# Kernel tuning notes

Hardware: AMD Instinct MI355X
Metric: run time of the kernel (lower is better)

The kernel has to match this reference:

```python
import jax, jax.numpy as jnp
import numpy as np
import math

D_HEAD = 64  # scaling uses sqrt(d_head), NOT sqrt of full projection dim (faithful to source)

def setup_inputs() -> dict:
    key = jax.random.key(0)
    ks = jax.random.split(key, 9)
    B, S, D = 4, 2048, 1024
    s = 0.02
    return {
        "x": jax.random.normal(ks[0], (B, S, D), dtype=jnp.float32),
        "Wq": jax.random.normal(ks[1], (D, D), dtype=jnp.float32) * s,
        "bq": jax.random.normal(ks[2], (D,), dtype=jnp.float32) * s,
        "Wk": jax.random.normal(ks[3], (D, D), dtype=jnp.float32) * s,
        "bk": jax.random.normal(ks[4], (D,), dtype=jnp.float32) * s,
        "Wv": jax.random.normal(ks[5], (D, D), dtype=jnp.float32) * s,
        "bv": jax.random.normal(ks[6], (D,), dtype=jnp.float32) * s,
        "Wo": jax.random.normal(ks[7], (D, D), dtype=jnp.float32) * s,
        "bo": jax.random.normal(ks[8], (D,), dtype=jnp.float32) * s,
    }

def reference(x, Wq, bq, Wk, bk, Wv, bv, Wo, bo):
    # Q/K/V projections: [B,S,D] @ [D,D] + b
    Q = jnp.einsum('bsd,de->bse', x, Wq) + bq
    K = jnp.einsum('bsd,de->bse', x, Wk) + bk
    V = jnp.einsum('bsd,de->bse', x, Wv) + bv
    # NOTE: source does bmm over the FULL projected dim (no head split),
    # scaled by sqrt(d_head) only.
    scores = jnp.einsum('bqd,bkd->bqk', Q, K) / math.sqrt(D_HEAD)  # [B,S,S]
    S_len = scores.shape[-1]
    causal = jnp.tril(jnp.ones((S_len, S_len), dtype=bool))
    scores = jnp.where(causal, scores, -jnp.inf)
    weights = jax.nn.softmax(scores, axis=-1)
    attn_out = jnp.einsum('bqk,bkd->bqd', weights, V)
    return jnp.einsum('bsd,de->bse', attn_out, Wo) + bo
```

## Files before the change

### kernel.cpp

```cpp
#include <hip/hip_runtime.h>
#include <stdint.h>

typedef _Float16 f16;
typedef __attribute__((ext_vector_type(8))) _Float16 f16x8;
typedef __attribute__((ext_vector_type(4))) _Float16 f16x4;
typedef __attribute__((ext_vector_type(4))) float f32x4;

typedef __attribute__((address_space(3))) uint32_t lds_u32;
typedef const __attribute__((address_space(1))) uint32_t glb_u32;

__device__ __forceinline__ void gload_lds16(const void* g, void* l) {
    __builtin_amdgcn_global_load_lds((glb_u32*)g, (lds_u32*)l, 16, 0, 0);
}


template<int ROWS>
__device__ __forceinline__
void stage2(const f16* __restrict__ G, int ldg, f16* lds,
            int grow0, int k0, int tid)
{
    const int l = tid & 63, w = tid >> 6;
    #pragma unroll
    for (int q = 0; q < ROWS / 32; ++q) {
        const int r = q * 32 + w * 8 + (l >> 3);
        const int csw = (((l & 7) ^ (r & 7)) << 3);
        gload_lds16(G + (long long)(grow0 + r) * ldg + (k0 + csw),
                    lds + q * 2048 + w * 512);
    }
}

template<int OUT_MODE, int CAUSAL, int TM, int TN>
__device__ __forceinline__
void gemm2_body(const f16* __restrict__ A, const f16* __restrict__ B,
                const float* __restrict__ bias, void* __restrict__ Cv,
                int M, int N, int K,
                long long sAb, long long sBb, long long sCb, float scale,
                int bx, int by, int bzi)
{
    constexpr int IM = TM / 32;
    constexpr int JN = TN / 32;

    int mtile, n0;
    if (CAUSAL == 1) {
        int rem = bx, mi = 0;
        while (rem > mi) { rem -= mi + 1; ++mi; }
        mtile = mi;
        n0 = rem * TN;
    } else {
        mtile = by;
        n0 = bx * TN;
    }

    const int tid  = threadIdx.x;
    const int wave = tid >> 6;
    const int lane = tid & 63;
    const long long bz = bzi;
    A += bz * sAb;
    B += bz * sBb;

    __shared__ f16 As[2][TM * 64];
    __shared__ f16 Bs[2][TN * 64];

    const int fr  = lane & 15;
    const int hk  = lane >> 4;
    const int lsw = lane & 7;
    const int wm  = (wave >> 1) * (TM / 2);
    const int wn  = (wave & 1) * (TN / 2);

    const int npass = (CAUSAL == 2) ? 2 : 1;
    for (int pass = 0; pass < npass; ++pass) {
        const int mt = (CAUSAL == 2 && pass == 1) ? (M / TM - 1 - mtile) : mtile;
        const int m0 = mt * TM;
        const int Kend = (CAUSAL == 2) ? (m0 + TM) : K;

        f32x4 acc[IM][JN] = {};

        stage2<TM>(A, K, &As[0][0], m0, 0, tid);
        stage2<TN>(B, K, &Bs[0][0], n0, 0, tid);
        asm volatile("s_waitcnt vmcnt(0)" ::: "memory");
        __builtin_amdgcn_s_barrier();

        int cur = 0;
        for (int k0 = 0; k0 < Kend; k0 += 64) {
            if (k0 + 64 < Kend) {
                stage2<TM>(A, K, &As[cur ^ 1][0], m0, k0 + 64, tid);
                stage2<TN>(B, K, &Bs[cur ^ 1][0], n0, k0 + 64, tid);
            }

            f16x8 af[IM][2], bf[JN][2];
            #pragma unroll
            for (int i = 0; i < IM; ++i)
                #pragma unroll
                for (int kk = 0; kk < 2; ++kk)
                    af[i][kk] = *(const f16x8*)((const char*)&As[cur][0] +
                        ((wm + i * 16 + fr) << 7) +
                        ((((kk << 2) | hk) ^ lsw) << 4));
            #pragma unroll
            for (int j = 0; j < JN; ++j)
                #pragma unroll
                for (int kk = 0; kk < 2; ++kk)
                    bf[j][kk] = *(const f16x8*)((const char*)&Bs[cur][0] +
                        ((wn + j * 16 + fr) << 7) +
                        ((((kk << 2) | hk) ^ lsw) << 4));

            asm volatile("s_waitcnt lgkmcnt(0)" ::: "memory");
            __builtin_amdgcn_s_setprio(1);
            #pragma unroll
            for (int i = 0; i < IM; ++i)
                #pragma unroll
                for (int j = 0; j < JN; ++j)
                    #pragma unroll
                    for (int kk = 0; kk < 2; ++kk)
                        acc[i][j] = __builtin_amdgcn_mfma_f32_16x16x32_f16(
                            af[i][kk], bf[j][kk], acc[i][j], 0, 0, 0);
            __builtin_amdgcn_s_setprio(0);

            asm volatile("s_waitcnt vmcnt(0)" ::: "memory");
            __builtin_amdgcn_s_barrier();
            cur ^= 1;
        }

        const int cn = lane & 15;
        const int cm = (lane >> 4) * 4;
        #pragma unroll
        for (int j = 0; j < JN; ++j) {
            const int gn = n0 + wn + j * 16 + cn;
            #pragma unroll
            for (int i = 0; i < IM; ++i) {
                const int gm = m0 + wm + i * 16 + cm;
                if (OUT_MODE == 0) {
                    const float bv = bias ? bias[gn] : 0.f;
                    float* C = (float*)Cv + bz * sCb;
                    #pragma unroll
                    for (int r = 0; r < 4; ++r)
                        C[(long long)(gm + r) * N + gn] = acc[i][j][r] * scale + bv;
                } else {
                    const float bv = bias ? bias[(long long)bz * N + gn] : 0.f;
                    f16* C = (f16*)Cv + bz * sCb;
                    #pragma unroll
                    for (int r = 0; r < 4; ++r)
                        C[(long long)(gm + r) * N + gn] = (f16)(acc[i][j][r] * scale + bv);
                }
            }
        }
    }
}

template<int OUT_MODE, int CAUSAL, int TM, int TN>
__global__ __launch_bounds__(256, 2)
void gemm2_bt(const f16* __restrict__ A, const f16* __restrict__ B,
              const float* __restrict__ bias, void* __restrict__ Cv,
              int M, int N, int K,
              long long sAb, long long sBb, long long sCb, float scale)
{
    gemm2_body<OUT_MODE, CAUSAL, TM, TN>(A, B, bias, Cv, M, N, K,
                                         sAb, sBb, sCb, scale,
                                         blockIdx.x, blockIdx.y, blockIdx.z);
}


__device__ __forceinline__
void stage_half(const f16* __restrict__ G, int ldg, f16* lds_half,
                int grow0, int k0, int tid)
{
    const int lr  = tid >> 3;
    const int csw = ((tid & 7) * 8) ^ ((lr & 7) << 3);
    gload_lds16(G + (long long)(grow0 + lr) * ldg + (k0 + csw),
                lds_half + ((tid >> 6) << 9));
    gload_lds16(G + (long long)(grow0 + 64 + lr) * ldg + (k0 + csw),
                lds_half + 4096 + ((tid >> 6) << 9));
}

template<int MODE>
__global__ __launch_bounds__(512, 2)
void gemm256_4ph(const f16* __restrict__ A, const f16* __restrict__ B,
                 const float* __restrict__ bias, const float* __restrict__ bias2,
                 f16* __restrict__ C0, f16* __restrict__ C1,
                 int M, int N, int K,
                 long long sAb, long long sBb, long long sCb, float scale)
{
    __shared__ f16 As[2][16384];
    __shared__ f16 Bs[2][16384];

    const int nwg  = gridDim.x;
    const int orig = blockIdx.x;
    const int swz  = (orig & 7) * (nwg >> 3) + (orig >> 3);

    int m0, n0;
    long long bz = 0;
    if (MODE == 1) {
        const int nr  = M >> 8;
        const int per = nr * (nr + 1) / 2;
        bz = swz / per;
        int rem = swz - (int)bz * per, mi = 0;
        while (rem > mi) { rem -= mi + 1; ++mi; }
        m0 = mi << 8;
        n0 = rem << 8;
    } else {
        const int ntn = N >> 8;
        const int mt = swz / ntn, nt = swz - mt * ntn;
        m0 = mt << 8;
        n0 = nt << 8;
    }
    A += bz * sAb;
    B += bz * sBb;

    const int tid  = threadIdx.x;
    const int lane = tid & 63;
    const int wave = tid >> 6;
    const int wm = (wave >> 2) << 7;
    const int wn = (wave & 3) << 6;
    const int fr  = lane & 15;
    const int hk  = lane >> 4;
    const int lsw = lane & 7;
    const int nkt = K >> 6;

    f32x4 acc[8][4] = {};
    f16x8 bf[4][2];

    stage_half(A, K, &As[0][0],    m0,       0, tid);
    stage_half(A, K, &As[0][8192], m0 + 128, 0, tid);
    stage_half(B, K, &Bs[0][0],    n0,       0, tid);
    stage_half(B, K, &Bs[0][8192], n0 + 128, 0, tid);
    if (nkt > 1) {
        stage_half(B, K, &Bs[1][0],    n0,       64, tid);
        stage_half(B, K, &Bs[1][8192], n0 + 128, 64, tid);
        asm volatile("s_waitcnt vmcnt(4)" ::: "memory");
    } else {
        asm volatile("s_waitcnt vmcnt(0)" ::: "memory");
    }
    __builtin_amdgcn_s_barrier();

    for (int t = 0; t < nkt; ++t) {
        const f16* Ab = As[t & 1];
        const f16* Bb = Bs[t & 1];
        #pragma unroll
        for (int p = 0; p < 4; ++p) {
            if (p == 0) {
                #pragma unroll
                for (int j = 0; j < 4; ++j)
                    #pragma unroll
                    for (int kk = 0; kk < 2; ++kk)
                        bf[j][kk] = *(const f16x8*)((const char*)Bb +
                            ((wn + j * 16 + fr) << 7) +
                            ((((kk << 2) | hk) ^ lsw) << 4));
            }
            f16x8 af[2][2];
            #pragma unroll
            for (int ii = 0; ii < 2; ++ii)
                #pragma unroll
                for (int kk = 0; kk < 2; ++kk)
                    af[ii][kk] = *(const f16x8*)((const char*)Ab +
                        ((wm + (2 * p + ii) * 16 + fr) << 7) +
                        ((((kk << 2) | hk) ^ lsw) << 4));

            if (p == 0 && t + 1 < nkt)
                stage_half(A, K, &As[(t + 1) & 1][0],    m0,       (t + 1) << 6, tid);
            if (p == 1 && t + 1 < nkt)
                stage_half(A, K, &As[(t + 1) & 1][8192], m0 + 128, (t + 1) << 6, tid);
            if (p == 2 && t + 2 < nkt)
                stage_half(B, K, &Bs[t & 1][0],          n0,       (t + 2) << 6, tid);
            if (p == 3 && t + 2 < nkt)
                stage_half(B, K, &Bs[t & 1][8192],       n0 + 128, (t + 2) << 6, tid);

            if (p == 0) asm volatile("s_waitcnt lgkmcnt(8)" ::: "memory");
            __builtin_amdgcn_s_barrier();
            asm volatile("s_waitcnt lgkmcnt(0)" ::: "memory");
            __builtin_amdgcn_s_setprio(1);
            #pragma unroll
            for (int ii = 0; ii < 2; ++ii)
                #pragma unroll
                for (int j = 0; j < 4; ++j)
                    #pragma unroll
                    for (int kk = 0; kk < 2; ++kk)
                        acc[2 * p + ii][j] = __builtin_amdgcn_mfma_f32_16x16x32_f16(
                            af[ii][kk], bf[j][kk], acc[2 * p + ii][j], 0, 0, 0);
            __builtin_amdgcn_s_setprio(0);
            if (p == 3) {
                if (t + 2 < nkt) asm volatile("s_waitcnt vmcnt(4)" ::: "memory");
                else             asm volatile("s_waitcnt vmcnt(0)" ::: "memory");
            }
            __builtin_amdgcn_s_barrier();
        }
    }

    const int cn  = lane & 15;
    const int cm4 = (lane >> 4) * 4;
    #pragma unroll
    for (int j = 0; j < 4; ++j) {
        const int gn = n0 + wn + j * 16 + cn;
        if (MODE == 3) {
            const int sel = gn >> 10;
            const int nn  = gn & 1023;
            #pragma unroll
            for (int i = 0; i < 8; ++i) {
                const int gm = m0 + wm + i * 16 + cm4;
                if (sel == 0) {
                    #pragma unroll
                    for (int r = 0; r < 4; ++r)
                        C0[(long long)(gm + r) * 1024 + nn] = (f16)acc[i][j][r];
                } else {
                    const float bb = bias2[nn];
                    const int b = gm >> 11, s = gm & 2047;
                    f16x4 pk;
                    #pragma unroll
                    for (int r = 0; r < 4; ++r)
                        pk[r] = (f16)(acc[i][j][r] + bb);
                    *(f16x4*)&C1[(long long)b * 2097152 + (long long)nn * 2048 + s] = pk;
                }
            }
        } else {
            const float cbv = bias ? bias[bz * N + gn] : 0.f;
            f16* Cc = C0 + bz * sCb;
            #pragma unroll
            for (int i = 0; i < 8; ++i) {
                const int gm = m0 + wm + i * 16 + cm4;
                #pragma unroll
                for (int r = 0; r < 4; ++r)
                    Cc[(long long)(gm + r) * N + gn] = (f16)(acc[i][j][r] * scale + cbv);
            }
        }
    }
}

__global__ __launch_bounds__(256)
void prep(const float* __restrict__ x,  const float* __restrict__ Wq,
          const float* __restrict__ bq, const float* __restrict__ Wk,
          const float* __restrict__ Wv, const float* __restrict__ bv,
          const float* __restrict__ Wo,
          f16* __restrict__ xb,  f16* __restrict__ Wqf, f16* __restrict__ Wkf,
          f16* __restrict__ Wvf, f16* __restrict__ Wot,
          float* __restrict__ bvo, float* __restrict__ wvec)
{
    __shared__ f16 tile[32][33];
    __shared__ float red[4][64];
    const int t = threadIdx.x;
    int id = blockIdx.x;

    if (id < 8192) {
        const int i = (id * 256 + t) * 4;
        const float4 v = *(const float4*)&x[i];
        f16x4 o; o[0]=(f16)v.x; o[1]=(f16)v.y; o[2]=(f16)v.z; o[3]=(f16)v.w;
        *(f16x4*)&xb[i] = o;
        return;
    }
    id -= 8192;
    if (id < 3072) {
        const float* src = (id < 1024) ? Wq : (id < 2048) ? Wk : Wv;
        f16* dst = (id < 1024) ? Wqf : (id < 2048) ? Wkf : Wvf;
        const int i = ((id & 1023) * 256 + t) * 4;
        const float4 v = *(const float4*)&src[i];
        f16x4 o; o[0]=(f16)v.x; o[1]=(f16)v.y; o[2]=(f16)v.z; o[3]=(f16)v.w;
        *(f16x4*)&dst[i] = o;
        return;
    }
    id -= 3072;
    if (id < 1024) {
        const int bx = (id & 31) * 32, by = (id >> 5) * 32;
        const int tx = t & 31, ty = t >> 5;
        #pragma unroll
        for (int i = 0; i < 32; i += 8)
            tile[ty + i][tx] = (f16)Wo[(long long)(by + ty + i) * 1024 + (bx + tx)];
        __syncthreads();
        #pragma unroll
        for (int i = 0; i < 32; i += 8)
            Wot[(long long)(bx + ty + i) * 1024 + (by + tx)] = tile[tx][ty + i];
        return;
    }
    id -= 1024;
    if (id < 16) {
        const int e0 = id * 64;
        const int wave = t >> 6, lane = t & 63;
        float a0 = 0.f, a1 = 0.f, a2 = 0.f, a3 = 0.f;
        for (int i = 0; i < 256; i += 4) {
            const int k = wave * 256 + i;
            a0 += bv[k]     * Wo[(long long)k * 1024 + e0 + lane];
            a1 += bv[k + 1] * Wo[(long long)(k + 1) * 1024 + e0 + lane];
            a2 += bv[k + 2] * Wo[(long long)(k + 2) * 1024 + e0 + lane];
            a3 += bv[k + 3] * Wo[(long long)(k + 3) * 1024 + e0 + lane];
        }
        red[wave][lane] = (a0 + a1) + (a2 + a3);
        __syncthreads();
        if (wave == 0)
            bvo[e0 + lane] = red[0][lane] + red[1][lane] + red[2][lane] + red[3][lane];
        return;
    }
    id -= 16;
    {
        const int row = id * 4 + (t >> 6);
        const int lane = t & 63;
        const float* src = Wk + (long long)row * 1024;
        float a = 0.f;
        #pragma unroll
        for (int tt = 0; tt < 16; ++tt) a += src[lane + 64 * tt] * bq[lane + 64 * tt];
        #pragma unroll
        for (int o = 32; o > 0; o >>= 1) a += __shfl_down(a, o);
        if (lane == 0) wvec[row] = a * 0.125f;
    }
}

__global__ __launch_bounds__(256, 2)
void dual_weights_cvec(const f16* __restrict__ Wkf, const f16* __restrict__ Wqf,
                       const f16* __restrict__ Wot, const f16* __restrict__ Wvf,
                       f16* __restrict__ Wcat2,
                       const f16* __restrict__ xb, const float* __restrict__ wvec,
                       float* __restrict__ cbias)
{
    if (blockIdx.z == 2) {
        const int flat = blockIdx.y * 8 + blockIdx.x;
        const int wave = threadIdx.x >> 6, lane = threadIdx.x & 63;
        #pragma unroll 4
        for (int rr = 0; rr < 32; ++rr) {
            const int row = (flat * 4 + wave) * 32 + rr;
            const f16* src = xb + (long long)row * 1024;
            float a = 0.f;
            #pragma unroll
            for (int tt = 0; tt < 16; ++tt)
                a += (float)src[lane + 64 * tt] * wvec[lane + 64 * tt];
            #pragma unroll
            for (int o = 32; o > 0; o >>= 1) a += __shfl_down(a, o);
            if (lane == 0) cbias[row] = a;
        }
        return;
    }
    const f16* Ax = (blockIdx.z == 0) ? Wkf : Wot;
    const f16* Bx = (blockIdx.z == 0) ? Wqf : Wvf;
    f16* Cx = Wcat2 + (long long)blockIdx.z * 1024 * 1024;
    gemm2_body<1, 0, 128, 128>(Ax, Bx, nullptr, Cx,
                               1024, 1024, 1024, 0, 0, 0, 1.f,
                               blockIdx.x, blockIdx.y, 0);
}

__global__ __launch_bounds__(256)
void softmax_causal(const f16* __restrict__ Sc, f16* __restrict__ P, int S)
{
    const long long row = blockIdx.x;
    const int q = (int)(row % S);
    const f16* src = Sc + row * S;
    f16* dst = P + row * S;
    const int t = threadIdx.x;
    __shared__ float redm[4], reds[4];

    f16x8 vv = {};
    if (t * 8 <= q) vv = *(const f16x8*)&src[t * 8];
    float v[8];
    float mx = -3.0e38f;
    #pragma unroll
    for (int i = 0; i < 8; ++i) {
        const int k = t * 8 + i;
        v[i] = (float)vv[i];
        if (k <= q) mx = fmaxf(mx, v[i]);
    }
    #pragma unroll
    for (int o = 32; o > 0; o >>= 1) mx = fmaxf(mx, __shfl_down(mx, o));
    if ((t & 63) == 0) redm[t >> 6] = mx;
    __syncthreads();
    mx = fmaxf(fmaxf(redm[0], redm[1]), fmaxf(redm[2], redm[3]));

    float sum = 0.f;
    #pragma unroll
    for (int i = 0; i < 8; ++i) {
        const int k = t * 8 + i;
        v[i] = (k <= q) ? __expf(v[i] - mx) : 0.f;
        sum += v[i];
    }
    #pragma unroll
    for (int o = 32; o > 0; o >>= 1) sum += __shfl_down(sum, o);
    if ((t & 63) == 0) reds[t >> 6] = sum;
    __syncthreads();
    sum = reds[0] + reds[1] + reds[2] + reds[3];
    const float inv = 1.f / sum;
    const int kend = ((q >> 7) + 1) << 7;
    if (t * 8 < kend) {
        f16x8 ov;
        #pragma unroll
        for (int i = 0; i < 8; ++i) ov[i] = (f16)(v[i] * inv);
        *(f16x8*)&dst[t * 8] = ov;
    }
}

extern "C" void kernel_launch(void* const* d_in, const int* in_sizes, int n_in,
                              void* d_out, int out_size, void* d_ws, size_t ws_size,
                              hipStream_t stream)
{
    const float* x  = (const float*)d_in[0];
    const float* Wq = (const float*)d_in[1];
    const float* bq = (const float*)d_in[2];
    const float* Wk = (const float*)d_in[3];
    const float* Wv = (const float*)d_in[5];
    const float* bv = (const float*)d_in[6];
    const float* Wo = (const float*)d_in[7];
    const float* bo = (const float*)d_in[8];
    float* out = (float*)d_out;

    const int B = 4, S = 2048, D = 1024;
    const long long SD  = (long long)S * D;
    const long long SS  = (long long)S * S;
    const long long BSD = (long long)B * SD;
    const int MS = B * S;

    char* p = (char*)d_ws;
    f16*   xb    = (f16*)p;  p += BSD * 2;
    f16*   Wqf   = (f16*)p;  p += (long long)D * D * 2;
    f16*   Wkf   = (f16*)p;  p += (long long)D * D * 2;
    f16*   Wvf   = (f16*)p;  p += (long long)D * D * 2;
    f16*   Wot   = (f16*)p;  p += (long long)D * D * 2;
    f16*   Wcat2 = (f16*)p;  p += 2LL * D * D * 2;
    float* bvo   = (float*)p; p += D * 4;
    float* wvec  = (float*)p; p += D * 4;
    float* cbias = (float*)p; p += (long long)MS * 4;
    f16*   Qh    = (f16*)p;  p += BSD * 2;
    f16*   Vt    = (f16*)p;  p += BSD * 2;
    f16*   Sc    = (f16*)p;  p += (long long)B * SS * 2;
    f16*   Pb    = (f16*)p;  p += (long long)B * SS * 2;

    dim3 blk(256);

    prep<<<dim3(12560), blk, 0, stream>>>(x, Wq, bq, Wk, Wv, bv, Wo,
                                          xb, Wqf, Wkf, Wvf, Wot, bvo, wvec);

    dual_weights_cvec<<<dim3(8, 8, 3), blk, 0, stream>>>(Wkf, Wqf, Wot, Wvf,
                                                         Wcat2, xb, wvec, cbias);

    dim3 gproj((MS / 256) * (2 * D / 256));
    gemm256_4ph<3><<<gproj, dim3(512), 0, stream>>>(xb, Wcat2, nullptr, bvo,
                                                    Qh, Vt,
                                                    MS, 2 * D, D, 0, 0, 0, 1.f);

    dim3 gsc(144);
    gemm256_4ph<1><<<gsc, dim3(512), 0, stream>>>(Qh, xb, cbias, nullptr,
                                                  Sc, nullptr,
                                                  S, S, D, SD, SD, SS, 0.125f);

    softmax_causal<<<dim3((unsigned)(B * S)), blk, 0, stream>>>(Sc, Pb, S);

    dim3 gpv(D / 64, S / 128 / 2, B);
    gemm2_bt<0, 2, 128, 64><<<gpv, blk, 0, stream>>>(Pb, Vt, bo, out,
                                                     S, D, S, SS, SD, SD, 1.f);
}
```

Measured before the change: 250.7 us.

## Fuse softmax normalization into PV GEMM using precomputed row statistics

The softmax kernel now computes only per-row max and reciprocal sum, one wave per row, and no longer writes a normalized probability matrix. The PV GEMM reads raw scores, applies exp, scaling and the causal mask while staging A tiles into LDS, and so drops the B*S*S f16 write and re-read of P. In exchange, A is loaded through registers instead of direct-to-LDS, each PV block repeats the exp work per N-tile, and the rowstat pass still reads the full score matrix.

```diff
diff --git a/kernel.cpp b/kernel.cpp
--- a/kernel.cpp
+++ b/kernel.cpp
@@ -146,18 +146,150 @@
     }
 }
 
-template<int OUT_MODE, int CAUSAL, int TM, int TN>
-__global__ __launch_bounds__(256, 2)
-void gemm2_bt(const f16* __restrict__ A, const f16* __restrict__ B,
-              const float* __restrict__ bias, void* __restrict__ Cv,
-              int M, int N, int K,
-              long long sAb, long long sBb, long long sCb, float scale)
-{
-    gemm2_body<OUT_MODE, CAUSAL, TM, TN>(A, B, bias, Cv, M, N, K,
-                                         sAb, sBb, sCb, scale,
-                                         blockIdx.x, blockIdx.y, blockIdx.z);
-}
-
+
+__device__ __forceinline__
+void pv_loadA(const f16* __restrict__ A, int lda, int m0, int k0, int tid,
+              f16x8 va[4])
+{
+    const int l = tid & 63, w = tid >> 6;
+    #pragma unroll
+    for (int q = 0; q < 4; ++q) {
+        const int r = q * 32 + w * 8 + (l >> 3);
+        const int csw = (((l & 7) ^ (r & 7)) << 3);
+        va[q] = *(const f16x8*)&A[(long long)(m0 + r) * lda + (k0 + csw)];
+    }
+}
+
+__device__ __forceinline__
+void pv_writeA(f16* lds, const f16x8 va[4], const float2 st[4],
+               int m0, int k0, int tid)
+{
+    const int l = tid & 63, w = tid >> 6;
+    #pragma unroll
+    for (int q = 0; q < 4; ++q) {
+        const int r = q * 32 + w * 8 + (l >> 3);
+        const int qrow = m0 + r;
+        const int csw = (((l & 7) ^ (r & 7)) << 3);
+        f16x8 o;
+        #pragma unroll
+        for (int e = 0; e < 8; ++e) {
+            const int k = k0 + csw + e;
+            const float p = (k <= qrow)
+                ? __expf((float)va[q][e] - st[q].x) * st[q].y : 0.f;
+            o[e] = (f16)p;
+        }
+        *(f16x8*)&lds[q * 2048 + w * 512 + l * 8] = o;
+    }
+}
+
+__global__ __launch_bounds__(256, 3)
+void pv_fused(const f16* __restrict__ Sc, const f16* __restrict__ Vt,
+              const float2* __restrict__ rs, const float* __restrict__ bo,
+              float* __restrict__ out)
+{
+    constexpr int S = 2048, D = 1024;
+    constexpr int TM = 128, TN = 64, IM = 4, JN = 2;
+    const int tid  = threadIdx.x;
+    const int wave = tid >> 6;
+    const int lane = tid & 63;
+    const long long bz = blockIdx.z;
+    const f16* A  = Sc + bz * ((long long)S * S);
+    const f16* Bp = Vt + bz * ((long long)D * S);
+    const float2* rsb = rs + bz * S;
+    const int n0 = blockIdx.x * TN;
+    const int mtile = blockIdx.y;
+
+    __shared__ f16 As[2][TM * 64];
+    __shared__ f16 Bs[2][TN * 64];
+
+    const int fr  = lane & 15;
+    const int hk  = lane >> 4;
+    const int lsw = lane & 7;
+    const int wm  = (wave >> 1) * (TM / 2);
+    const int wn  = (wave & 1) * (TN / 2);
+    const int w8  = (tid >> 6) * 8 + ((tid & 63) >> 3);
+
+    for (int pass = 0; pass < 2; ++pass) {
+        const int mt = (pass == 1) ? (S / TM - 1 - mtile) : mtile;
+        const int m0 = mt * TM;
+        const int Kend = m0 + TM;
+
+        float2 st[4];
+        #pragma unroll
+        for (int q = 0; q < 4; ++q) st[q] = rsb[m0 + q * 32 + w8];
+
+        f32x4 acc[IM][JN] = {};
+        f16x8 va[4];
+
+        pv_loadA(A, S, m0, 0, tid, va);
+        stage2<TN>(Bp, S, &Bs[0][0], n0, 0, tid);
+        asm volatile("s_waitcnt vmcnt(2)" ::: "memory");
+        pv_writeA(&As[0][0], va, st, m0, 0, tid);
+        asm volatile("s_waitcnt vmcnt(0) lgkmcnt(0)" ::: "memory");
+        __builtin_amdgcn_s_barrier();
+
+        int cur = 0;
+        for (int k0 = 0; k0 < Kend; k0 += 64) {
+            const bool nxt = (k0 + 64 < Kend);
+            if (nxt) {
+                pv_loadA(A, S, m0, k0 + 64, tid, va);
+                stage2<TN>(Bp, S, &Bs[cur ^ 1][0], n0, k0 + 64, tid);
+            }
+
+            f16x8 af[IM][2], bf[JN][2];
+            #pragma unroll
+            for (int i = 0; i < IM; ++i)
+                #pragma unroll
+                for (int kk = 0; kk < 2; ++kk)
+                    af[i][kk] = *(const f16x8*)((const char*)&As[cur][0] +
+                        ((wm + i * 16 + fr) << 7) +
+                        ((((kk << 2) | hk) ^ lsw) << 4));
+            #pragma unroll
+            for (int j = 0; j < JN; ++j)
+                #pragma unroll
+                for (int kk = 0; kk < 2; ++kk)
+                    bf[j][kk] = *(const f16x8*)((const char*)&Bs[cur][0] +
+                        ((wn + j * 16 + fr) << 7) +
+                        ((((kk << 2) | hk) ^ lsw) << 4));
+
+            asm volatile("s_waitcnt lgkmcnt(0)" ::: "memory");
+            __builtin_amdgcn_s_setprio(1);
+            #pragma unroll
+            for (int i = 0; i < IM; ++i)
+                #pragma unroll
+                for (int j = 0; j < JN; ++j)
+                    #pragma unroll
+                    for (int kk = 0; kk < 2; ++kk)
+                        acc[i][j] = __builtin_amdgcn_mfma_f32_16x16x32_f16(
+                            af[i][kk], bf[j][kk], acc[i][j], 0, 0, 0);
+            __builtin_amdgcn_s_setprio(0);
+
+            if (nxt) {
+                asm volatile("s_waitcnt vmcnt(2)" ::: "memory");
+                pv_writeA(&As[cur ^ 1][0], va, st, m0, k0 + 64, tid);
+            }
+            asm volatile("s_waitcnt vmcnt(0) lgkmcnt(0)" ::: "memory");
+            __builtin_amdgcn_s_barrier();
+            cur ^= 1;
+        }
+
+        const int cn = lane & 15;
+        const int cm = (lane >> 4) * 4;
+        float* C = out + bz * ((long long)S * D);
+        #pragma unroll
+        for (int j = 0; j < JN; ++j) {
+            const int gn = n0 + wn + j * 16 + cn;
+            const float bv = bo[gn];
+            #pragma unroll
+            for (int i = 0; i < IM; ++i) {
+                const int gm = m0 + wm + i * 16 + cm;
+                #pragma unroll
+                for (int r = 0; r < 4; ++r)
+                    C[(long long)(gm + r) * D + gn] = acc[i][j][r] + bv;
+            }
+        }
+    }
+}
 
 __device__ __forceinline__
 void stage_half(const f16* __restrict__ G, int ldg, f16* lds_half,
@@ -432,51 +564,44 @@
 }
 
 __global__ __launch_bounds__(256)
-void softmax_causal(const f16* __restrict__ Sc, f16* __restrict__ P, int S)
-{
-    const long long row = blockIdx.x;
-    const int q = (int)(row % S);
+void rowstat(const f16* __restrict__ Sc, float2* __restrict__ rs, int S)
+{
+    const int wave = threadIdx.x >> 6, lane = threadIdx.x & 63;
+    const long long row = (long long)blockIdx.x * 4 + wave;
+    const int q = (int)(row & (S - 1));
     const f16* src = Sc + row * S;
-    f16* dst = P + row * S;
-    const int t = threadIdx.x;
-    __shared__ float redm[4], reds[4];
-
-    f16x8 vv = {};
-    if (t * 8 <= q) vv = *(const f16x8*)&src[t * 8];
-    float v[8];
+
+    float v[32];
     float mx = -3.0e38f;
     #pragma unroll
-    for (int i = 0; i < 8; ++i) {
-        const int k = t * 8 + i;
-        v[i] = (float)vv[i];
-        if (k <= q) mx = fmaxf(mx, v[i]);
-    }
-    #pragma unroll
-    for (int o = 32; o > 0; o >>= 1) mx = fmaxf(mx, __shfl_down(mx, o));
-    if ((t & 63) == 0) redm[t >> 6] = mx;
-    __syncthreads();
-    mx = fmaxf(fmaxf(redm[0], redm[1]), fmaxf(redm[2], redm[3]));
+    for (int i = 0; i < 4; ++i) {
+        const int c0 = i * 512 + lane * 8;
+        f16x8 vv = {};
+        if (c0 <= q) vv = *(const f16x8*)&src[c0];
+        #pragma unroll
+        for (int e = 0; e < 8; ++e) {
+            const int k = c0 + e;
+            v[i * 8 + e] = (float)vv[e];
+            if (k <= q) mx = fmaxf(mx, v[i * 8 + e]);
+        }
+    }
+    #pragma unroll
+    for (int o = 32; o > 0; o >>= 1) mx = fmaxf(mx, __shfl_xor(mx, o));
 
     float sum = 0.f;
     #pragma unroll
-    for (int i = 0; i < 8; ++i) {
-        const int k = t * 8 + i;
-        v[i] = (k <= q) ? __expf(v[i] - mx) : 0.f;
-        sum += v[i];
-    }
-    #pragma unroll
-    for (int o = 32; o > 0; o >>= 1) sum += __shfl_down(sum, o);
-    if ((t & 63) == 0) reds[t >> 6] = sum;
-    __syncthreads();
-    sum = reds[0] + reds[1] + reds[2] + reds[3];
-    const float inv = 1.f / sum;
-    const int kend = ((q >> 7) + 1) << 7;
-    if (t * 8 < kend) {
-        f16x8 ov;
-        #pragma unroll
-        for (int i = 0; i < 8; ++i) ov[i] = (f16)(v[i] * inv);
-        *(f16x8*)&dst[t * 8] = ov;
-    }
+    for (int i = 0; i < 4; ++i) {
+        const int c0 = i * 512 + lane * 8;
+        #pragma unroll
+        for (int e = 0; e < 8; ++e) {
+            const int k = c0 + e;
+            if (k <= q) sum += __expf(v[i * 8 + e] - mx);
+        }
+    }
+    #pragma unroll
+    for (int o = 32; o > 0; o >>= 1) sum += __shfl_xor(sum, o);
+
+    if (lane == 0) rs[row] = make_float2(mx, 1.f / sum);
 }
 
 extern "C" void kernel_launch(void* const* d_in, const int* in_sizes, int n_in,
@@ -512,7 +637,7 @@
     f16*   Qh    = (f16*)p;  p += BSD * 2;
     f16*   Vt    = (f16*)p;  p += BSD * 2;
     f16*   Sc    = (f16*)p;  p += (long long)B * SS * 2;
-    f16*   Pb    = (f16*)p;  p += (long long)B * SS * 2;
+    float2* rs   = (float2*)p; p += (long long)MS * 8;
 
     dim3 blk(256);
 
@@ -532,9 +657,8 @@
                                                   Sc, nullptr,
                                                   S, S, D, SD, SD, SS, 0.125f);
 
-    softmax_causal<<<dim3((unsigned)(B * S)), blk, 0, stream>>>(Sc, Pb, S);
+    rowstat<<<dim3((unsigned)(B * S / 4)), blk, 0, stream>>>(Sc, rs, S);
 
     dim3 gpv(D / 64, S / 128 / 2, B);
-    gemm2_bt<0, 2, 128, 64><<<gpv, blk, 0, stream>>>(Pb, Vt, bo, out,
-                                                     S, D, S, SS, SD, SD, 1.f);
-}
+    pv_fused<<<gpv, blk, 0, stream>>>(Sc, Vt, rs, bo, out);
+}
```

New measurement: 285.0 us. +13.7%, slower.
